# Performance work log

Measured on AMD Instinct MI355X. Metric: run time of the kernel, lower is better.

## Reference

```python
import jax, jax.numpy as jnp
import numpy as np


def setup_inputs() -> dict:
    key = jax.random.key(0)
    k1, k2, k3 = jax.random.split(key, 3)
    bs, chart_len, H = 256, 1024, 256
    num_steps, start_index = 512, 512
    chart = jax.random.normal(k1, (bs, chart_len, 2 * H), dtype=jnp.float32)
    operations = jax.random.randint(k2, (num_steps, bs, 2), 0, start_index, dtype=jnp.int64)
    U = jax.random.normal(k3, (5 * H, 2 * H), dtype=jnp.float32) * 0.05
    b = jnp.zeros((5 * H,), dtype=jnp.float32)
    return {"chart": chart, "operations": operations, "start_index": start_index, "U": U, "b": b}


def reference(chart, operations, start_index, U, b):
    H = U.shape[0] // 5
    bs = chart.shape[0]
    batch_idx = jnp.arange(bs)
    num_steps = operations.shape[0]

    def step_fn(ch, xs):
        step, ops = xs
        left = ch[batch_idx, ops[:, 0]]   # [bs, 2H]
        right = ch[batch_idx, ops[:, 1]]  # [bs, 2H]
        ccL, ccR = left[:, :H], right[:, :H]
        hh = jnp.concatenate([left[:, H:], right[:, H:]], axis=-1)  # [bs, 2H]
        preact = hh @ U.T + b  # [bs, 5H]
        i = jax.nn.sigmoid(preact[:, :H])
        fL = jax.nn.sigmoid(preact[:, H:2 * H])
        fR = jax.nn.sigmoid(preact[:, 2 * H:3 * H])
        o = jax.nn.sigmoid(preact[:, 3 * H:4 * H])
        u = jnp.tanh(preact[:, 4 * H:5 * H])
        c = fL * ccL + fR * ccR + i * u
        h = o * jnp.tanh(c)
        ch = ch.at[:, start_index + step, :].set(jnp.concatenate([c, h], axis=-1))
        return ch, None

    chart, _ = jax.lax.scan(step_fn, chart, (jnp.arange(num_steps), operations))
    return chart
```

## Files before the change

kernel.cpp:

```cpp
#include <hip/hip_runtime.h>
#include <hip/hip_bf16.h>

#define H_     256
#define TWOH_  512
#define CL_    1024
#define BS_    256
#define START_ 512

typedef float  f32x16   __attribute__((ext_vector_type(16)));
typedef short  short8_t __attribute__((ext_vector_type(8)));
typedef short  short4_t __attribute__((ext_vector_type(4)));
typedef __bf16 bf16x8   __attribute__((ext_vector_type(8)));

static __device__ __forceinline__ unsigned short f2bf(float x) {
  __hip_bfloat16 h = __float2bfloat16(x);
  return __builtin_bit_cast(unsigned short, h);
}

static __device__ __forceinline__ void gload16(const void* g, void* l) {
  __builtin_amdgcn_global_load_lds(
      (const __attribute__((address_space(1))) void*)g,
      (__attribute__((address_space(3))) void*)l, 16, 0, 0);
}

#define SCHED0() __builtin_amdgcn_sched_barrier(0)

__global__ void uconv2_kernel(const float* __restrict__ U,
                              unsigned short* __restrict__ ubF) {
  int c = blockIdx.x * 256 + threadIdx.x;
  if (c >= 81920) return;
  int lane = c & 63;
  int t1 = c >> 6;
  int ks = t1 & 3;
  int t2 = t1 >> 2;
  int kt = t2 & 7;
  int t3 = t2 >> 3;
  int g  = t3 % 5;
  int jw = t3 / 5;
  int jc = jw >> 1, wn = jw & 1;
  int n  = g * 256 + jc * 64 + wn * 32 + (lane & 31);
  int k  = kt * 64 + (ks * 2 + (lane >> 5)) * 8;
  const float* src = U + (size_t)n * 512 + k;
  float4 f0 = *(const float4*)(src);
  float4 f1 = *(const float4*)(src + 4);
  short8_t v;
  v[0] = (short)f2bf(f0.x); v[1] = (short)f2bf(f0.y);
  v[2] = (short)f2bf(f0.z); v[3] = (short)f2bf(f0.w);
  v[4] = (short)f2bf(f1.x); v[5] = (short)f2bf(f1.y);
  v[6] = (short)f2bf(f1.z); v[7] = (short)f2bf(f1.w);
  *(short8_t*)(ubF + (size_t)c * 8) = v;
}

__global__ void hbcopy_kernel(const float4* __restrict__ chart4,
                              float4* __restrict__ out4,
                              unsigned short* __restrict__ hb) {
  const long long total = 16777216LL;
  long long tid = (long long)blockIdx.x * blockDim.x + threadIdx.x;
  for (long long e = tid; e < total; e += (long long)gridDim.x * blockDim.x) {
    long long i   = e >> 16;
    long long rem = e & 65535;
    long long off = (i << 17) + rem;
    float4 f = chart4[off];
    out4[off] = f;
    int col4 = (int)(rem & 127);
    if (col4 >= 64) {
      long long pos = rem >> 7;
      short4_t v;
      v[0] = (short)f2bf(f.x); v[1] = (short)f2bf(f.y);
      v[2] = (short)f2bf(f.z); v[3] = (short)f2bf(f.w);
      *(short4_t*)(hb + ((i * 512 + pos) * 256 + (long long)(col4 - 64) * 4)) = v;
    }
  }
}

__global__ void copy_kernel(const float4* __restrict__ src,
                            float4* __restrict__ dst) {
  long long tid = (long long)blockIdx.x * blockDim.x + threadIdx.x;
  const long long total = 16777216LL;
  for (long long e = tid; e < total; e += (long long)gridDim.x * blockDim.x) {
    long long i   = e >> 16;
    long long rem = e & 65535;
    long long off = (i << 17) + rem;
    dst[off] = src[off];
  }
}

__global__ __launch_bounds__(128) void chart6_kernel(
    const float* __restrict__ chart,
    const int* __restrict__ ops,
    const unsigned short* __restrict__ ubF,
    const unsigned short* __restrict__ hb,
    const float* __restrict__ bias,
    float* __restrict__ out)
{
  __shared__ unsigned short As[2][64 * 64];
  __shared__ int opsl[128];

  const int tid = threadIdx.x, lane = tid & 63, wn = tid >> 6;
  const int l31 = lane & 31, lhi = lane >> 5;

  const int bx = blockIdx.x;
  const int g  = (bx & 7) * 1024 + (bx >> 3);
  const int s  = g >> 4, mg = (g >> 2) & 3, jc = g & 3;

  opsl[tid] = ops[((size_t)s * BS_ + mg * 64) * 2 + tid];
  __syncthreads();

  const int chunkA = (tid & 7) ^ ((tid >> 3) & 7);
  int opL256[4], opR256[4];
  const unsigned short* hbA[4];
  #pragma unroll
  for (int p = 0; p < 4; ++p) {
    int rl = p * 16 + (tid >> 3);
    opL256[p] = opsl[2 * rl] * 256;
    opR256[p] = opsl[2 * rl + 1] * 256;
    hbA[p] = hb + ((size_t)(mg * 64 + rl) * 512) * 256 + chunkA * 8;
  }

  const unsigned short* bpB[5];
  #pragma unroll
  for (int p = 0; p < 5; ++p) {
    bpB[p] = ubF + ((size_t)(((jc * 2 + wn) * 5 + p) * 2048 + lane)) * 8;
  }

  f32x16 acc0[5], acc1[5];
  #pragma unroll
  for (int gg = 0; gg < 5; ++gg)
    #pragma unroll
    for (int q = 0; q < 16; ++q) { acc0[gg][q] = 0.f; acc1[gg][q] = 0.f; }

#define STAGE(BUF, KT) do {                                                     \
    const int koff_ = ((KT) < 4) ? (KT) * 64 : (KT) * 64 - 256;                 \
    _Pragma("unroll")                                                           \
    for (int p = 0; p < 4; ++p) {                                               \
      const unsigned short* g_ =                                                \
          hbA[p] + (((KT) < 4) ? opL256[p] : opR256[p]) + koff_;                \
      gload16(g_, &As[BUF][(p * 128 + tid) * 8]);                               \
    }                                                                           \
  } while (0)

  const int aro0 = l31 * 64;
  const int aro1 = (32 + l31) * 64;
  const int sw7  = l31 & 7;

#define COMPUTE(BUF, KT) do {                                                   \
    _Pragma("unroll")                                                           \
    for (int ks = 0; ks < 4; ++ks) {                                            \
      const int ce = ((ks * 2 + lhi) ^ sw7) * 8;                                \
      bf16x8 a0 = __builtin_bit_cast(bf16x8,                                    \
          *(const short8_t*)&As[BUF][aro0 + ce]);                               \
      bf16x8 a1 = __builtin_bit_cast(bf16x8,                                    \
          *(const short8_t*)&As[BUF][aro1 + ce]);                               \
      _Pragma("unroll")                                                         \
      for (int gg = 0; gg < 5; ++gg) {                                          \
        bf16x8 b = __builtin_bit_cast(bf16x8,                                   \
            *(const short8_t*)(bpB[gg] + ((KT) * 4 + ks) * 512));               \
        acc0[gg] = __builtin_amdgcn_mfma_f32_32x32x16_bf16(a0,b,acc0[gg],0,0,0);\
        acc1[gg] = __builtin_amdgcn_mfma_f32_32x32x16_bf16(a1,b,acc1[gg],0,0,0);\
      }                                                                         \
    }                                                                           \
  } while (0)

#define PHASE(BUF, KT, DOSTAGE) do {                                            \
    asm volatile("s_waitcnt vmcnt(4)" ::: "memory");                            \
    __builtin_amdgcn_s_barrier();                                               \
    SCHED0();                                                                   \
    COMPUTE(BUF, KT);                                                           \
    SCHED0();                                                                   \
    __builtin_amdgcn_s_barrier();                                               \
    SCHED0();                                                                   \
    if (DOSTAGE) { STAGE(BUF, (KT) + 2); SCHED0(); }                            \
  } while (0)

  STAGE(0, 0); SCHED0();
  STAGE(1, 1); SCHED0();

  PHASE(0, 0, true);
  PHASE(1, 1, true);
  PHASE(0, 2, true);
  PHASE(1, 3, true);
  PHASE(0, 4, true);
  PHASE(1, 5, true);
  PHASE(0, 6, false);
  asm volatile("s_waitcnt vmcnt(0)" ::: "memory");
  __builtin_amdgcn_s_barrier();
  SCHED0();
  COMPUTE(1, 7);

#undef PHASE
#undef COMPUTE
#undef STAGE

  const int jlane = jc * 64 + wn * 32 + l31;
  float bg[5];
  #pragma unroll
  for (int gg = 0; gg < 5; ++gg) bg[gg] = bias[gg * H_ + jlane];

#define EPI(ACC, MF) do {                                                       \
    _Pragma("unroll")                                                           \
    for (int q = 0; q < 16; ++q) {                                              \
      const int rl_  = (MF) * 32 + (q & 3) + 8 * (q >> 2) + 4 * lhi;            \
      const int i_   = mg * 64 + rl_;                                           \
      const int opL_ = opsl[2 * rl_], opR_ = opsl[2 * rl_ + 1];                 \
      const float ccL_ = chart[((size_t)i_ * CL_ + opL_) * TWOH_ + jlane];      \
      const float ccR_ = chart[((size_t)i_ * CL_ + opR_) * TWOH_ + jlane];      \
      float pi_  = (ACC)[0][q] + bg[0];                                         \
      float pfL_ = (ACC)[1][q] + bg[1];                                         \
      float pfR_ = (ACC)[2][q] + bg[2];                                         \
      float po_  = (ACC)[3][q] + bg[3];                                         \
      float pu_  = (ACC)[4][q] + bg[4];                                         \
      float gi_  = 1.f / (1.f + __expf(-pi_));                                  \
      float gfL_ = 1.f / (1.f + __expf(-pfL_));                                 \
      float gfR_ = 1.f / (1.f + __expf(-pfR_));                                 \
      float go_  = 1.f / (1.f + __expf(-po_));                                  \
      float eu_  = __expf(2.f * pu_);                                           \
      float gu_  = 1.f - 2.f / (eu_ + 1.f);                                     \
      float c_   = gfL_ * ccL_ + gfR_ * ccR_ + gi_ * gu_;                       \
      float ec_  = __expf(2.f * c_);                                            \
      float th_  = 1.f - 2.f / (ec_ + 1.f);                                     \
      float h_   = go_ * th_;                                                   \
      float* orow_ = out + ((size_t)i_ * CL_ + START_ + s) * TWOH_;             \
      orow_[jlane]      = c_;                                                   \
      orow_[H_ + jlane] = h_;                                                   \
    }                                                                           \
  } while (0)

  EPI(acc0, 0);
  EPI(acc1, 1);
#undef EPI
}

__global__ __launch_bounds__(256, 2) void chart1_kernel(
    const float* __restrict__ chart,
    const int* __restrict__ ops,
    const float* __restrict__ U,
    const float* __restrict__ bias,
    float* __restrict__ out)
{
  __shared__ unsigned short As[64 * 72];
  __shared__ unsigned short Bs[320 * 72];
  __shared__ int opsl[128];

  const int tid = threadIdx.x, lane = tid & 63, wid = tid >> 6;
  const int wm = wid & 1, wn = wid >> 1;
  const int bx = blockIdx.x, jc = blockIdx.y;
  const int s = bx >> 2, ibase = (bx & 3) * 64, j0 = jc * 64;

  if (tid < 128) opsl[tid] = ops[(s * BS_ + ibase) * 2 + tid];
  __syncthreads();

  const int arow = tid >> 2, aqc = tid & 3;
  const int opL_s = opsl[2 * arow], opR_s = opsl[2 * arow + 1];
  const long long abase_i = (long long)(ibase + arow) * CL_;

  f32x16 acc[5];
  #pragma unroll
  for (int g = 0; g < 5; ++g)
    #pragma unroll
    for (int q = 0; q < 16; ++q) acc[g][q] = 0.0f;

  const int a_off  = (wm * 32 + (lane & 31)) * 72 + 8 * (lane >> 5);
  const int b_off0 = (wn * 32 + (lane & 31)) * 72 + 8 * (lane >> 5);

  for (int kt = 0; kt < 8; ++kt) {
    const int k0 = kt * 64;
    {
      const int op   = (k0 < 256) ? opL_s : opR_s;
      const int col0 = ((k0 < 256) ? 256 + k0 : k0) + aqc * 16;
      const float* src = chart + (abase_i + op) * TWOH_ + col0;
      float4 f0 = *(const float4*)(src + 0);
      float4 f1 = *(const float4*)(src + 4);
      float4 f2 = *(const float4*)(src + 8);
      float4 f3 = *(const float4*)(src + 12);
      short8_t v0, v1;
      v0[0] = (short)f2bf(f0.x); v0[1] = (short)f2bf(f0.y);
      v0[2] = (short)f2bf(f0.z); v0[3] = (short)f2bf(f0.w);
      v0[4] = (short)f2bf(f1.x); v0[5] = (short)f2bf(f1.y);
      v0[6] = (short)f2bf(f1.z); v0[7] = (short)f2bf(f1.w);
      v1[0] = (short)f2bf(f2.x); v1[1] = (short)f2bf(f2.y);
      v1[2] = (short)f2bf(f2.z); v1[3] = (short)f2bf(f2.w);
      v1[4] = (short)f2bf(f3.x); v1[5] = (short)f2bf(f3.y);
      v1[6] = (short)f2bf(f3.z); v1[7] = (short)f2bf(f3.w);
      *(short8_t*)&As[arow * 72 + aqc * 16]     = v0;
      *(short8_t*)&As[arow * 72 + aqc * 16 + 8] = v1;
    }
    #pragma unroll
    for (int cc = 0; cc < 20; ++cc) {
      int chunk = cc * 256 + tid;
      int c  = chunk >> 4;
      int ko = (chunk & 15) * 4;
      int n  = ((c >> 6) << 8) + j0 + (c & 63);
      float4 f = *(const float4*)(U + (long long)n * 512 + k0 + ko);
      short4_t v;
      v[0] = (short)f2bf(f.x); v[1] = (short)f2bf(f.y);
      v[2] = (short)f2bf(f.z); v[3] = (short)f2bf(f.w);
      *(short4_t*)&Bs[c * 72 + ko] = v;
    }
    __syncthreads();

    #pragma unroll
    for (int ks = 0; ks < 4; ++ks) {
      bf16x8 a = __builtin_bit_cast(bf16x8, *(const short8_t*)&As[a_off + ks * 16]);
      #pragma unroll
      for (int g = 0; g < 5; ++g) {
        bf16x8 b = __builtin_bit_cast(bf16x8,
            *(const short8_t*)&Bs[b_off0 + g * 64 * 72 + ks * 16]);
        acc[g] = __builtin_amdgcn_mfma_f32_32x32x16_bf16(a, b, acc[g], 0, 0, 0);
      }
    }
    __syncthreads();
  }

  const int jlane = j0 + wn * 32 + (lane & 31);
  float bg[5];
  #pragma unroll
  for (int g = 0; g < 5; ++g) bg[g] = bias[g * H_ + jlane];

  #pragma unroll
  for (int q = 0; q < 16; ++q) {
    int rl  = wm * 32 + (q & 3) + 8 * (q >> 2) + 4 * (lane >> 5);
    int i   = ibase + rl;
    int opL = opsl[2 * rl], opR = opsl[2 * rl + 1];
    float ccL = chart[((long long)i * CL_ + opL) * TWOH_ + jlane];
    float ccR = chart[((long long)i * CL_ + opR) * TWOH_ + jlane];
    float pi  = acc[0][q] + bg[0];
    float pfL = acc[1][q] + bg[1];
    float pfR = acc[2][q] + bg[2];
    float po  = acc[3][q] + bg[3];
    float pu  = acc[4][q] + bg[4];
    float gi  = 1.f / (1.f + __expf(-pi));
    float gfL = 1.f / (1.f + __expf(-pfL));
    float gfR = 1.f / (1.f + __expf(-pfR));
    float go  = 1.f / (1.f + __expf(-po));
    float eu  = __expf(2.f * pu);
    float gu  = 1.f - 2.f / (eu + 1.f);
    float c   = gfL * ccL + gfR * ccR + gi * gu;
    float ec  = __expf(2.f * c);
    float th  = 1.f - 2.f / (ec + 1.f);
    float h   = go * th;
    float* orow = out + ((long long)i * CL_ + START_ + s) * TWOH_;
    orow[jlane]      = c;
    orow[H_ + jlane] = h;
  }
}

extern "C" void kernel_launch(void* const* d_in, const int* in_sizes, int n_in,
                              void* d_out, int out_size, void* d_ws, size_t ws_size,
                              hipStream_t stream) {
  const float* chart = (const float*)d_in[0];
  const int*   ops   = (const int*)d_in[1];
  const float* U     = (const float*)d_in[3];
  const float* bias  = (const float*)d_in[4];
  float* out = (float*)d_out;

  const size_t HB_OFF   = (size_t)2 << 20;
  const size_t HB_BYTES = (size_t)256 * 512 * 256 * 2;

  if (ws_size >= HB_OFF + HB_BYTES) {
    unsigned short* ubF = (unsigned short*)d_ws;
    unsigned short* hb  = (unsigned short*)((char*)d_ws + HB_OFF);
    uconv2_kernel<<<320, 256, 0, stream>>>(U, ubF);
    hbcopy_kernel<<<4096, 256, 0, stream>>>((const float4*)chart, (float4*)out, hb);
    chart6_kernel<<<8192, 128, 0, stream>>>(chart, ops, ubF, hb, bias, out);
  } else {
    copy_kernel<<<4096, 256, 0, stream>>>((const float4*)chart, (float4*)out);
    chart1_kernel<<<dim3(2048, 4), 256, 0, stream>>>(chart, ops, U, bias, out);
  }
}
```

Baseline: 472.4 us.

## Halve LSTM GEMM row tile and interleave gate weights for occupancy

Cuts each block's M tile from 64 to 32 rows and doubles the grid. This halves the accumulator registers and staged LDS per block, and adds a launch bound of four blocks per CU to raise occupancy for latency hiding. The bf16 U layout is reordered so the five gates sit next to each other, letting a single base pointer address all B fragments. In exchange, each B fragment now feeds one MFMA instead of two, so weight traffic from cache doubles.

```diff
diff --git a/kernel.cpp b/kernel.cpp
--- a/kernel.cpp
+++ b/kernel.cpp
@@ -25,18 +25,17 @@
 
 #define SCHED0() __builtin_amdgcn_sched_barrier(0)
 
-__global__ void uconv2_kernel(const float* __restrict__ U,
+__global__ void uconv3_kernel(const float* __restrict__ U,
                               unsigned short* __restrict__ ubF) {
   int c = blockIdx.x * 256 + threadIdx.x;
   if (c >= 81920) return;
   int lane = c & 63;
-  int t1 = c >> 6;
-  int ks = t1 & 3;
-  int t2 = t1 >> 2;
-  int kt = t2 & 7;
-  int t3 = t2 >> 3;
-  int g  = t3 % 5;
-  int jw = t3 / 5;
+  int f  = c >> 6;
+  int g  = f % 5;
+  int t  = f / 5;
+  int ks = t & 3;
+  int kt = (t >> 2) & 7;
+  int jw = t >> 5;
   int jc = jw >> 1, wn = jw & 1;
   int n  = g * 256 + jc * 64 + wn * 32 + (lane & 31);
   int k  = kt * 64 + (ks * 2 + (lane >> 5)) * 8;
@@ -85,7 +84,7 @@
   }
 }
 
-__global__ __launch_bounds__(128) void chart6_kernel(
+__global__ __launch_bounds__(128, 4) void chart7_kernel(
     const float* __restrict__ chart,
     const int* __restrict__ ops,
     const unsigned short* __restrict__ ubF,
@@ -93,76 +92,72 @@
     const float* __restrict__ bias,
     float* __restrict__ out)
 {
-  __shared__ unsigned short As[2][64 * 64];
-  __shared__ int opsl[128];
+  __shared__ unsigned short As[2][32 * 64];
+  __shared__ int opsl[64];
 
   const int tid = threadIdx.x, lane = tid & 63, wn = tid >> 6;
   const int l31 = lane & 31, lhi = lane >> 5;
 
-  const int bx = blockIdx.x;
-  const int g  = (bx & 7) * 1024 + (bx >> 3);
-  const int s  = g >> 4, mg = (g >> 2) & 3, jc = g & 3;
-
-  opsl[tid] = ops[((size_t)s * BS_ + mg * 64) * 2 + tid];
+  const int bx  = blockIdx.x;
+  const int g   = (bx & 7) * 2048 + (bx >> 3);
+  const int s   = g >> 5;
+  const int sub = g & 31;
+  const int mg  = sub >> 2;
+  const int jc  = sub & 3;
+
+  if (tid < 64) opsl[tid] = ops[((size_t)s * BS_ + mg * 32) * 2 + tid];
   __syncthreads();
 
   const int chunkA = (tid & 7) ^ ((tid >> 3) & 7);
-  int opL256[4], opR256[4];
-  const unsigned short* hbA[4];
-  #pragma unroll
-  for (int p = 0; p < 4; ++p) {
+  int opL256[2], opR256[2];
+  const unsigned short* hbA[2];
+  #pragma unroll
+  for (int p = 0; p < 2; ++p) {
     int rl = p * 16 + (tid >> 3);
     opL256[p] = opsl[2 * rl] * 256;
     opR256[p] = opsl[2 * rl + 1] * 256;
-    hbA[p] = hb + ((size_t)(mg * 64 + rl) * 512) * 256 + chunkA * 8;
-  }
-
-  const unsigned short* bpB[5];
-  #pragma unroll
-  for (int p = 0; p < 5; ++p) {
-    bpB[p] = ubF + ((size_t)(((jc * 2 + wn) * 5 + p) * 2048 + lane)) * 8;
-  }
-
-  f32x16 acc0[5], acc1[5];
+    hbA[p] = hb + ((size_t)(mg * 32 + rl) * 512) * 256 + chunkA * 8;
+  }
+
+  const unsigned short* bpB =
+      ubF + ((size_t)((jc * 2 + wn) * 160 + 2)) * 512 + lane * 8;
+
+  f32x16 acc[5];
   #pragma unroll
   for (int gg = 0; gg < 5; ++gg)
     #pragma unroll
-    for (int q = 0; q < 16; ++q) { acc0[gg][q] = 0.f; acc1[gg][q] = 0.f; }
+    for (int q = 0; q < 16; ++q) acc[gg][q] = 0.f;
 
 #define STAGE(BUF, KT) do {                                                     \
     const int koff_ = ((KT) < 4) ? (KT) * 64 : (KT) * 64 - 256;                 \
     _Pragma("unroll")                                                           \
-    for (int p = 0; p < 4; ++p) {                                               \
+    for (int p = 0; p < 2; ++p) {                                               \
       const unsigned short* g_ =                                                \
           hbA[p] + (((KT) < 4) ? opL256[p] : opR256[p]) + koff_;                \
       gload16(g_, &As[BUF][(p * 128 + tid) * 8]);                               \
     }                                                                           \
   } while (0)
 
-  const int aro0 = l31 * 64;
-  const int aro1 = (32 + l31) * 64;
-  const int sw7  = l31 & 7;
+  const int sw7 = l31 & 7;
+  const int aro = l31 * 64;
 
 #define COMPUTE(BUF, KT) do {                                                   \
     _Pragma("unroll")                                                           \
     for (int ks = 0; ks < 4; ++ks) {                                            \
       const int ce = ((ks * 2 + lhi) ^ sw7) * 8;                                \
-      bf16x8 a0 = __builtin_bit_cast(bf16x8,                                    \
-          *(const short8_t*)&As[BUF][aro0 + ce]);                               \
-      bf16x8 a1 = __builtin_bit_cast(bf16x8,                                    \
-          *(const short8_t*)&As[BUF][aro1 + ce]);                               \
+      bf16x8 a = __builtin_bit_cast(bf16x8,                                     \
+          *(const short8_t*)&As[BUF][aro + ce]);                                \
       _Pragma("unroll")                                                         \
       for (int gg = 0; gg < 5; ++gg) {                                          \
         bf16x8 b = __builtin_bit_cast(bf16x8,                                   \
-            *(const short8_t*)(bpB[gg] + ((KT) * 4 + ks) * 512));               \
-        acc0[gg] = __builtin_amdgcn_mfma_f32_32x32x16_bf16(a0,b,acc0[gg],0,0,0);\
-        acc1[gg] = __builtin_amdgcn_mfma_f32_32x32x16_bf16(a1,b,acc1[gg],0,0,0);\
+            *(const short8_t*)(bpB + (((KT) * 4 + ks) * 5 + gg - 2) * 512));    \
+        acc[gg] = __builtin_amdgcn_mfma_f32_32x32x16_bf16(a, b, acc[gg],0,0,0); \
       }                                                                         \
     }                                                                           \
   } while (0)
 
 #define PHASE(BUF, KT, DOSTAGE) do {                                            \
-    asm volatile("s_waitcnt vmcnt(4)" ::: "memory");                            \
+    asm volatile("s_waitcnt vmcnt(2)" ::: "memory");                            \
     __builtin_amdgcn_s_barrier();                                               \
     SCHED0();                                                                   \
     COMPUTE(BUF, KT);                                                           \
@@ -196,38 +191,32 @@
   #pragma unroll
   for (int gg = 0; gg < 5; ++gg) bg[gg] = bias[gg * H_ + jlane];
 
-#define EPI(ACC, MF) do {                                                       \
-    _Pragma("unroll")                                                           \
-    for (int q = 0; q < 16; ++q) {                                              \
-      const int rl_  = (MF) * 32 + (q & 3) + 8 * (q >> 2) + 4 * lhi;            \
-      const int i_   = mg * 64 + rl_;                                           \
-      const int opL_ = opsl[2 * rl_], opR_ = opsl[2 * rl_ + 1];                 \
-      const float ccL_ = chart[((size_t)i_ * CL_ + opL_) * TWOH_ + jlane];      \
-      const float ccR_ = chart[((size_t)i_ * CL_ + opR_) * TWOH_ + jlane];      \
-      float pi_  = (ACC)[0][q] + bg[0];                                         \
-      float pfL_ = (ACC)[1][q] + bg[1];                                         \
-      float pfR_ = (ACC)[2][q] + bg[2];                                         \
-      float po_  = (ACC)[3][q] + bg[3];                                         \
-      float pu_  = (ACC)[4][q] + bg[4];                                         \
-      float gi_  = 1.f / (1.f + __expf(-pi_));                                  \
-      float gfL_ = 1.f / (1.f + __expf(-pfL_));                                 \
-      float gfR_ = 1.f / (1.f + __expf(-pfR_));                                 \
-      float go_  = 1.f / (1.f + __expf(-po_));                                  \
-      float eu_  = __expf(2.f * pu_);                                           \
-      float gu_  = 1.f - 2.f / (eu_ + 1.f);                                     \
-      float c_   = gfL_ * ccL_ + gfR_ * ccR_ + gi_ * gu_;                       \
-      float ec_  = __expf(2.f * c_);                                            \
-      float th_  = 1.f - 2.f / (ec_ + 1.f);                                     \
-      float h_   = go_ * th_;                                                   \
-      float* orow_ = out + ((size_t)i_ * CL_ + START_ + s) * TWOH_;             \
-      orow_[jlane]      = c_;                                                   \
-      orow_[H_ + jlane] = h_;                                                   \
-    }                                                                           \
-  } while (0)
-
-  EPI(acc0, 0);
-  EPI(acc1, 1);
-#undef EPI
+  #pragma unroll
+  for (int q = 0; q < 16; ++q) {
+    const int rl  = (q & 3) + 8 * (q >> 2) + 4 * lhi;
+    const int i   = mg * 32 + rl;
+    const int opL = opsl[2 * rl], opR = opsl[2 * rl + 1];
+    const float ccL = chart[((size_t)i * CL_ + opL) * TWOH_ + jlane];
+    const float ccR = chart[((size_t)i * CL_ + opR) * TWOH_ + jlane];
+    float pi  = acc[0][q] + bg[0];
+    float pfL = acc[1][q] + bg[1];
+    float pfR = acc[2][q] + bg[2];
+    float po  = acc[3][q] + bg[3];
+    float pu  = acc[4][q] + bg[4];
+    float gi  = 1.f / (1.f + __expf(-pi));
+    float gfL = 1.f / (1.f + __expf(-pfL));
+    float gfR = 1.f / (1.f + __expf(-pfR));
+    float go  = 1.f / (1.f + __expf(-po));
+    float eu  = __expf(2.f * pu);
+    float gu  = 1.f - 2.f / (eu + 1.f);
+    float c   = gfL * ccL + gfR * ccR + gi * gu;
+    float ec  = __expf(2.f * c);
+    float th  = 1.f - 2.f / (ec + 1.f);
+    float h   = go * th;
+    float* orow = out + ((size_t)i * CL_ + START_ + s) * TWOH_;
+    orow[jlane]      = c;
+    orow[H_ + jlane] = h;
+  }
 }
 
 __global__ __launch_bounds__(256, 2) void chart1_kernel(
@@ -359,9 +348,9 @@
   if (ws_size >= HB_OFF + HB_BYTES) {
     unsigned short* ubF = (unsigned short*)d_ws;
     unsigned short* hb  = (unsigned short*)((char*)d_ws + HB_OFF);
-    uconv2_kernel<<<320, 256, 0, stream>>>(U, ubF);
+    uconv3_kernel<<<320, 256, 0, stream>>>(U, ubF);
     hbcopy_kernel<<<4096, 256, 0, stream>>>((const float4*)chart, (float4*)out, hb);
-    chart6_kernel<<<8192, 128, 0, stream>>>(chart, ops, ubF, hb, bias, out);
+    chart7_kernel<<<16384, 128, 0, stream>>>(chart, ops, ubF, hb, bias, out);
   } else {
     copy_kernel<<<4096, 256, 0, stream>>>((const float4*)chart, (float4*)out);
     chart1_kernel<<<dim3(2048, 4), 256, 0, stream>>>(chart, ops, U, bias, out);
```

Result: slower. 563.2 us (+19.2%).
